# Kernel tuning notes

Measured on AMD Instinct MI355X. Metric: run time of the kernel, lower is better.

Reference implementation:

```python
import jax, jax.numpy as jnp
import numpy as np

N = 1_000_000
C = 64
B = 64
GRID = (256, 256, 256)
LEVELS = [(1, 1, 1), (2, 2, 2), (4, 4, 4), (4, 4, 8)]
NBINS_TOTAL = sum(nx * ny * nz for nx, ny, nz in LEVELS)  # 201


def setup_inputs() -> dict:
    key = jax.random.key(0)
    ks = jax.random.split(key, 12)
    feats = jax.random.normal(ks[0], (N, C), dtype=jnp.float32)
    batch_indices = jax.random.randint(ks[1], (N,), 0, B, dtype=jnp.int32)
    voxel_coords = jax.random.randint(ks[2], (N, 3), 0, 256, dtype=jnp.int32)
    s = lambda k, sh, fan: jax.random.normal(k, sh, dtype=jnp.float32) / np.sqrt(fan)
    return {
        "feats": feats,
        "batch_indices": batch_indices,
        "voxel_coords": voxel_coords,
        "batch_size": B,
        "aW1": s(ks[3], (C, 32), C), "ab1": jnp.zeros((32,), jnp.float32),
        "aW2": s(ks[4], (32, 1), 32), "ab2": jnp.zeros((1,), jnp.float32),
        "pW1": s(ks[5], (C * NBINS_TOTAL, 256), C * NBINS_TOTAL), "pb1": jnp.zeros((256,), jnp.float32),
        "pW2": s(ks[6], (256, 256), 256), "pb2": jnp.zeros((256,), jnp.float32),
    }


def _event_softmax(s, batch_indices, batch_size):
    # s: [N] raw attention scores; softmax within each event
    smax = jax.ops.segment_max(s, batch_indices, num_segments=batch_size)
    sexp = jnp.exp(s - smax[batch_indices])
    ssum = jax.ops.segment_sum(sexp, batch_indices, num_segments=batch_size)
    return sexp / (ssum[batch_indices] + 1e-8)


def reference(feats, batch_indices, voxel_coords, batch_size,
              aW1, ab1, aW2, ab2, pW1, pb1, pW2, pb2):
    # attention MLP -> per-voxel scalar score
    h = jax.nn.relu(feats @ aW1 + ab1)
    raw = (h @ aW2 + ab2)[:, 0]                       # [N]
    attn = _event_softmax(raw, batch_indices, batch_size)  # [N]
    weighted = feats * attn[:, None]                  # [N, C]

    cx = voxel_coords[:, 0].astype(jnp.float32)
    cy = voxel_coords[:, 1].astype(jnp.float32)
    cz = voxel_coords[:, 2].astype(jnp.float32)

    level_pools = []
    for nx, ny, nz in LEVELS:
        bx = jnp.clip((cx / GRID[0] * nx).astype(jnp.int32), 0, nx - 1)
        by = jnp.clip((cy / GRID[1] * ny).astype(jnp.int32), 0, ny - 1)
        bz = jnp.clip((cz / GRID[2] * nz).astype(jnp.int32), 0, nz - 1)
        bin_id = batch_indices * (nx * ny * nz) + bx * (ny * nz) + by * nz + bz
        n_bins = batch_size * nx * ny * nz
        sums = jax.ops.segment_sum(weighted, bin_id, num_segments=n_bins)      # [n_bins, C]
        counts = jax.ops.segment_sum(jnp.ones_like(bin_id, dtype=jnp.float32), bin_id,
                                     num_segments=n_bins)                      # [n_bins]
        pooled = jnp.where(counts[:, None] > 0, sums / jnp.maximum(counts, 1.0)[:, None], 0.0)
        level_pools.append(pooled.reshape(batch_size, nx * ny * nz * weighted.shape[1]))

    pyramid = jnp.concatenate(level_pools, axis=-1)   # [B, C * 201]
    return jax.nn.relu(pyramid @ pW1 + pb1) @ pW2 + pb2
```

## Files before the change

kernel.cpp:

```cpp
#include <hip/hip_runtime.h>

#define NPTS 1000000
#define C 64
#define B 64
#define NFINE 128
#define KTOT (64*201)
#define SREP 532480
#define LSTRIDE 65

typedef float f32x4 __attribute__((ext_vector_type(4)));


__global__ __launch_bounds__(256)
void zero_kernel(float4* __restrict__ p, int nf4) {
    int i = blockIdx.x * 256 + threadIdx.x;
    if (i < nf4) p[i] = make_float4(0.f, 0.f, 0.f, 0.f);
}

__global__ __launch_bounds__(256)
void fused_kernel(const float* __restrict__ feats,
                  const int* __restrict__ bidx,
                  const int* __restrict__ coords,
                  const float* __restrict__ aW1,
                  const float* __restrict__ ab1,
                  const float* __restrict__ aW2,
                  const float* __restrict__ ab2,
                  float* __restrict__ wsbase,
                  int rmask,
                  float* __restrict__ ESUM) {
    __shared__ float sh_es[B];
    __shared__ float lds_w[256 * LSTRIDE];
    float* __restrict__ S   = wsbase + (size_t)(blockIdx.x & rmask) * SREP;
    float* __restrict__ cnt = S + 524288;
    const int tid = threadIdx.x;
    const int lane = tid & 63;
    const int wv = tid >> 6;
    if (tid < B) sh_es[tid] = 0.f;
    __syncthreads();

    const int ntiles = (NPTS + 255) / 256;
    for (int tile = blockIdx.x; tile < ntiles; tile += gridDim.x) {
        const int p = tile * 256 + tid;
        int mybin = -1;
        if (p < NPTS) {
            f32x4 r[16];
            const f32x4* fr = (const f32x4*)(feats + (size_t)p * C);
            #pragma unroll
            for (int i = 0; i < 16; ++i) r[i] = __builtin_nontemporal_load(&fr[i]);
            float h[32];
            #pragma unroll
            for (int j = 0; j < 32; ++j) h[j] = ab1[j];
            #pragma unroll
            for (int i = 0; i < 16; ++i) {
                const float f0 = r[i].x, f1 = r[i].y, f2 = r[i].z, f3 = r[i].w;
                #pragma unroll
                for (int j = 0; j < 32; ++j) {
                    h[j] = fmaf(f0, aW1[(4*i+0)*32 + j],
                           fmaf(f1, aW1[(4*i+1)*32 + j],
                           fmaf(f2, aW1[(4*i+2)*32 + j],
                           fmaf(f3, aW1[(4*i+3)*32 + j], h[j]))));
                }
            }
            float raw = ab2[0];
            #pragma unroll
            for (int j = 0; j < 32; ++j) raw = fmaf(fmaxf(h[j], 0.f), aW2[j], raw);
            const float e = expf(raw);
            const int b = __builtin_nontemporal_load(&bidx[p]);
            const int cx = __builtin_nontemporal_load(&coords[3*p]);
            const int cy = __builtin_nontemporal_load(&coords[3*p+1]);
            const int cz = __builtin_nontemporal_load(&coords[3*p+2]);
            mybin = b * NFINE + ((cx >> 6) << 5) + ((cy >> 6) << 3) + (cz >> 5);
            atomicAdd(&sh_es[b], e);
            float* wr = &lds_w[tid * LSTRIDE];
            #pragma unroll
            for (int i = 0; i < 16; ++i) {
                wr[4*i+0] = r[i].x * e;
                wr[4*i+1] = r[i].y * e;
                wr[4*i+2] = r[i].z * e;
                wr[4*i+3] = r[i].w * e;
            }
        }
        #pragma unroll
        for (int q = 0; q < 64; ++q) {
            const int bq = __shfl(mybin, q);
            if (bq >= 0) {
                const float v = lds_w[(wv * 64 + q) * LSTRIDE + lane];
                atomicAdd(&S[(size_t)bq * C + lane], v);
            }
        }
        if (mybin >= 0) atomicAdd(&cnt[mybin], 1.0f);
    }
    __syncthreads();
    if (tid < B) atomicAdd(&ESUM[tid], sh_es[tid]);
}

__global__ __launch_bounds__(256)
void finalize_kernel(const float* __restrict__ wsbase, int R,
                     const float* __restrict__ ESUM, float* __restrict__ P) {
    __shared__ float sS[NFINE * C];
    __shared__ float sc[NFINE];
    const int b = blockIdx.x;
    const int tid = threadIdx.x;
    for (int i = tid; i < NFINE * C; i += 256) {
        float s = 0.f;
        for (int r = 0; r < R; ++r) s += wsbase[(size_t)r * SREP + (size_t)b * NFINE * C + i];
        sS[i] = s;
    }
    for (int i = tid; i < NFINE; i += 256) {
        float s = 0.f;
        for (int r = 0; r < R; ++r) s += wsbase[(size_t)r * SREP + 524288 + b * NFINE + i];
        sc[i] = s;
    }
    __syncthreads();
    const float inv_es = 1.0f / ESUM[b];
    float* Pb = P + (size_t)b * KTOT;
    const int lane = tid & 63;
    const int wv = tid >> 6;
    for (int bin = wv; bin < 128; bin += 4) {
        const float c = sc[bin];
        Pb[4672 + bin*C + lane] = (c > 0.f) ? sS[bin*C + lane] * inv_es / fmaxf(c, 1.f) : 0.f;
    }
    for (int bin = wv; bin < 64; bin += 4) {
        const int x = bin >> 4, y = (bin >> 2) & 3, z = bin & 3;
        const int f0 = x*32 + y*8 + 2*z;
        const float c = sc[f0] + sc[f0 + 1];
        const float s = sS[f0*C + lane] + sS[(f0+1)*C + lane];
        Pb[576 + bin*C + lane] = (c > 0.f) ? s * inv_es / fmaxf(c, 1.f) : 0.f;
    }
    for (int bin = wv; bin < 8; bin += 4) {
        const int x = bin >> 2, y = (bin >> 1) & 1, z = bin & 1;
        float c = 0.f, s = 0.f;
        for (int dx = 0; dx < 2; ++dx)
            for (int dy = 0; dy < 2; ++dy)
                for (int dz = 0; dz < 4; ++dz) {
                    const int f = (2*x+dx)*32 + (2*y+dy)*8 + (4*z+dz);
                    c += sc[f]; s += sS[f*C + lane];
                }
        Pb[64 + bin*C + lane] = (c > 0.f) ? s * inv_es / fmaxf(c, 1.f) : 0.f;
    }
    if (wv == 0) {
        float c = 0.f, s = 0.f;
        for (int f = 0; f < 128; ++f) { c += sc[f]; s += sS[f*C + lane]; }
        Pb[lane] = (c > 0.f) ? s * inv_es / fmaxf(c, 1.f) : 0.f;
    }
}

__global__ __launch_bounds__(256)
void gemm1_kernel(const float* __restrict__ P, const float* __restrict__ W1,
                  float* __restrict__ acc) {
    __shared__ float sP[64 * 128];
    const int jb = blockIdx.x;
    const int kb = blockIdx.y;
    const int k0 = kb * 128;
    const int kw = min(128, KTOT - k0);
    const int tid = threadIdx.x;
    for (int i = tid; i < 64 * 32; i += 256) {
        const int row = i >> 5, c4 = i & 31;
        if (c4 * 4 < kw)
            *(float4*)&sP[row*128 + c4*4] =
                *(const float4*)&P[(size_t)row * KTOT + k0 + c4*4];
    }
    __syncthreads();
    const int j = jb * 64 + (tid & 63);
    const int g = tid >> 6;
    float a[16];
    #pragma unroll
    for (int i = 0; i < 16; ++i) a[i] = 0.f;
    for (int k4 = 0; k4 < (kw >> 2); ++k4) {
        const int k = 4 * k4;
        const float w0 = W1[(size_t)(k0+k+0)*256 + j];
        const float w1 = W1[(size_t)(k0+k+1)*256 + j];
        const float w2 = W1[(size_t)(k0+k+2)*256 + j];
        const float w3 = W1[(size_t)(k0+k+3)*256 + j];
        #pragma unroll
        for (int i = 0; i < 16; ++i) {
            const float4 pv = *(const float4*)&sP[(g + 4*i)*128 + k];
            a[i] = fmaf(pv.x, w0, fmaf(pv.y, w1, fmaf(pv.z, w2, fmaf(pv.w, w3, a[i]))));
        }
    }
    #pragma unroll
    for (int i = 0; i < 16; ++i)
        atomicAdd(&acc[(g + 4*i)*256 + j], a[i]);
}

__global__ __launch_bounds__(256)
void gemm2_kernel(const float* __restrict__ acc, const float* __restrict__ pb1,
                  const float* __restrict__ W2, const float* __restrict__ pb2,
                  float* __restrict__ out) {
    __shared__ float R[256];
    const int b = blockIdx.x, j = threadIdx.x;
    R[j] = fmaxf(acc[b*256 + j] + pb1[j], 0.f);
    __syncthreads();
    float s = pb2[j];
    #pragma unroll 8
    for (int m = 0; m < 256; ++m) s = fmaf(R[m], W2[m*256 + j], s);
    out[b*256 + j] = s;
}

extern "C" void kernel_launch(void* const* d_in, const int* in_sizes, int n_in,
                              void* d_out, int out_size, void* d_ws, size_t ws_size,
                              hipStream_t stream) {
    const float* feats  = (const float*)d_in[0];
    const int*   bidx   = (const int*)d_in[1];
    const int*   coords = (const int*)d_in[2];
    const float* aW1 = (const float*)d_in[4];
    const float* ab1 = (const float*)d_in[5];
    const float* aW2 = (const float*)d_in[6];
    const float* ab2 = (const float*)d_in[7];
    const float* pW1 = (const float*)d_in[8];
    const float* pb1 = (const float*)d_in[9];
    const float* pW2 = (const float*)d_in[10];
    const float* pb2 = (const float*)d_in[11];
    float* out = (float*)d_out;
    float* ws  = (float*)d_ws;

    int R = 8;
    while (R > 1 && ((size_t)R * SREP + 16448 + 823296) * 4 > ws_size) R >>= 1;

    float* ESUM = ws + (size_t)R * SREP;
    float* acc1 = ESUM + 64;
    float* Pyr  = acc1 + 16384;

    const int zf4 = R * (SREP / 4) + 16448 / 4;
    hipLaunchKernelGGL(zero_kernel, dim3((zf4 + 255) / 256), dim3(256), 0, stream,
                       (float4*)ws, zf4);
    hipLaunchKernelGGL(fused_kernel, dim3(2048), dim3(256), 0, stream,
                       feats, bidx, coords, aW1, ab1, aW2, ab2, ws, R - 1, ESUM);
    hipLaunchKernelGGL(finalize_kernel, dim3(64), dim3(256), 0, stream, ws, R, ESUM, Pyr);
    hipLaunchKernelGGL(gemm1_kernel, dim3(4, 101), dim3(256), 0, stream, Pyr, pW1, acc1);
    hipLaunchKernelGGL(gemm2_kernel, dim3(64), dim3(256), 0, stream, acc1, pb1, pW2, pb2, out);
}
```

Baseline: 807.9 us.

## Pick scatter replica by XCC ID and use workgroup-scope atomics

When eight replicas are available, the fused kernel reads the hardware XCC ID and picks the partial-sum replica private to that chiplet. It then issues relaxed workgroup-scope float atomics, so the adds can resolve in that XCC's L2 instead of at device coherence scope. The LDS staging buffer is also halved by processing each wavefront's 64 points in two 32-point halves, which lowers shared-memory use per block and may allow more resident blocks. The risk is correctness: it relies on all blocks of one XCC sharing an L2 and on results being written back at kernel end.

```diff
diff --git a/kernel.cpp b/kernel.cpp
--- a/kernel.cpp
+++ b/kernel.cpp
@@ -17,6 +17,7 @@
     if (i < nf4) p[i] = make_float4(0.f, 0.f, 0.f, 0.f);
 }
 
+template<int LOCAL>
 __global__ __launch_bounds__(256)
 void fused_kernel(const float* __restrict__ feats,
                   const int* __restrict__ bidx,
@@ -29,8 +30,16 @@
                   int rmask,
                   float* __restrict__ ESUM) {
     __shared__ float sh_es[B];
-    __shared__ float lds_w[256 * LSTRIDE];
-    float* __restrict__ S   = wsbase + (size_t)(blockIdx.x & rmask) * SREP;
+    __shared__ float lds_w[128 * LSTRIDE];
+    int rep;
+    if (LOCAL) {
+        unsigned int xcc;
+        asm volatile("s_getreg_b32 %0, hwreg(HW_REG_XCC_ID)" : "=s"(xcc));
+        rep = (int)(xcc & 7u);
+    } else {
+        rep = blockIdx.x & rmask;
+    }
+    float* __restrict__ S   = wsbase + (size_t)rep * SREP;
     float* __restrict__ cnt = S + 524288;
     const int tid = threadIdx.x;
     const int lane = tid & 63;
@@ -42,8 +51,9 @@
     for (int tile = blockIdx.x; tile < ntiles; tile += gridDim.x) {
         const int p = tile * 256 + tid;
         int mybin = -1;
+        f32x4 r[16];
+        float e = 0.f;
         if (p < NPTS) {
-            f32x4 r[16];
             const f32x4* fr = (const f32x4*)(feats + (size_t)p * C);
             #pragma unroll
             for (int i = 0; i < 16; ++i) r[i] = __builtin_nontemporal_load(&fr[i]);
@@ -64,31 +74,46 @@
             float raw = ab2[0];
             #pragma unroll
             for (int j = 0; j < 32; ++j) raw = fmaf(fmaxf(h[j], 0.f), aW2[j], raw);
-            const float e = expf(raw);
+            e = expf(raw);
             const int b = __builtin_nontemporal_load(&bidx[p]);
             const int cx = __builtin_nontemporal_load(&coords[3*p]);
             const int cy = __builtin_nontemporal_load(&coords[3*p+1]);
             const int cz = __builtin_nontemporal_load(&coords[3*p+2]);
             mybin = b * NFINE + ((cx >> 6) << 5) + ((cy >> 6) << 3) + (cz >> 5);
             atomicAdd(&sh_es[b], e);
-            float* wr = &lds_w[tid * LSTRIDE];
-            #pragma unroll
-            for (int i = 0; i < 16; ++i) {
-                wr[4*i+0] = r[i].x * e;
-                wr[4*i+1] = r[i].y * e;
-                wr[4*i+2] = r[i].z * e;
-                wr[4*i+3] = r[i].w * e;
+        }
+        #pragma unroll
+        for (int sub = 0; sub < 2; ++sub) {
+            if (mybin >= 0 && (lane >> 5) == sub) {
+                float* wr = &lds_w[(wv * 32 + (lane & 31)) * LSTRIDE];
+                #pragma unroll
+                for (int i = 0; i < 16; ++i) {
+                    wr[4*i+0] = r[i].x * e;
+                    wr[4*i+1] = r[i].y * e;
+                    wr[4*i+2] = r[i].z * e;
+                    wr[4*i+3] = r[i].w * e;
+                }
             }
-        }
-        #pragma unroll
-        for (int q = 0; q < 64; ++q) {
-            const int bq = __shfl(mybin, q);
-            if (bq >= 0) {
-                const float v = lds_w[(wv * 64 + q) * LSTRIDE + lane];
-                atomicAdd(&S[(size_t)bq * C + lane], v);
+            #pragma unroll
+            for (int q = 0; q < 32; ++q) {
+                const int bq = __shfl(mybin, sub * 32 + q);
+                if (bq >= 0) {
+                    const float v = lds_w[(wv * 32 + q) * LSTRIDE + lane];
+                    if (LOCAL)
+                        __hip_atomic_fetch_add(&S[(size_t)bq * C + lane], v,
+                                               __ATOMIC_RELAXED, __HIP_MEMORY_SCOPE_WORKGROUP);
+                    else
+                        atomicAdd(&S[(size_t)bq * C + lane], v);
+                }
             }
         }
-        if (mybin >= 0) atomicAdd(&cnt[mybin], 1.0f);
+        if (mybin >= 0) {
+            if (LOCAL)
+                __hip_atomic_fetch_add(&cnt[mybin], 1.0f,
+                                       __ATOMIC_RELAXED, __HIP_MEMORY_SCOPE_WORKGROUP);
+            else
+                atomicAdd(&cnt[mybin], 1.0f);
+        }
     }
     __syncthreads();
     if (tid < B) atomicAdd(&ESUM[tid], sh_es[tid]);
@@ -224,8 +249,12 @@
     const int zf4 = R * (SREP / 4) + 16448 / 4;
     hipLaunchKernelGGL(zero_kernel, dim3((zf4 + 255) / 256), dim3(256), 0, stream,
                        (float4*)ws, zf4);
-    hipLaunchKernelGGL(fused_kernel, dim3(2048), dim3(256), 0, stream,
-                       feats, bidx, coords, aW1, ab1, aW2, ab2, ws, R - 1, ESUM);
+    if (R == 8)
+        hipLaunchKernelGGL((fused_kernel<1>), dim3(2048), dim3(256), 0, stream,
+                           feats, bidx, coords, aW1, ab1, aW2, ab2, ws, 7, ESUM);
+    else
+        hipLaunchKernelGGL((fused_kernel<0>), dim3(2048), dim3(256), 0, stream,
+                           feats, bidx, coords, aW1, ab1, aW2, ab2, ws, R - 1, ESUM);
     hipLaunchKernelGGL(finalize_kernel, dim3(64), dim3(256), 0, stream, ws, R, ESUM, Pyr);
     hipLaunchKernelGGL(gemm1_kernel, dim3(4, 101), dim3(256), 0, stream, Pyr, pW1, acc1);
     hipLaunchKernelGGL(gemm2_kernel, dim3(64), dim3(256), 0, stream, acc1, pb1, pW2, pb2, out);
```

New measurement: 808.3 us. About the same (+0.1%).

## Replace atomic scatter pooling with counting-sort by bin and segmented gather-reduce

Applied to the files above, without the earlier changes.

The fused MLP-plus-atomic-scatter kernel is split up. An MLP pass writes each point's exp score and fine bin id. A histogram, three scan kernels and a placement kernel then counting-sort the point indices by bin, and a gather kernel reduces each bin's features with no atomics. This removes the heavy global float atomics and the replicated accumulation buffers. In exchange it adds a second random-access read of the 256MB feats array, several small serial kernels (a single-block scan, 64-block hist/place), and extra launches.

```diff
diff --git a/kernel.cpp b/kernel.cpp
--- a/kernel.cpp
+++ b/kernel.cpp
@@ -3,114 +3,187 @@
 #define NPTS 1000000
 #define C 64
 #define B 64
-#define NFINE 128
+#define NBINS 8192
 #define KTOT (64*201)
-#define SREP 532480
-#define LSTRIDE 65
+#define NSLICE 64
+#define SLICE 15625
+#define A 1048576
 
 typedef float f32x4 __attribute__((ext_vector_type(4)));
 
-
-__global__ __launch_bounds__(256)
-void zero_kernel(float4* __restrict__ p, int nf4) {
+#define ZOFF (4*A + 1056800)
+
+__global__ __launch_bounds__(256)
+void zero_kernel(float4* __restrict__ p) {
     int i = blockIdx.x * 256 + threadIdx.x;
-    if (i < nf4) p[i] = make_float4(0.f, 0.f, 0.f, 0.f);
-}
-
-__global__ __launch_bounds__(256)
-void fused_kernel(const float* __restrict__ feats,
-                  const int* __restrict__ bidx,
-                  const int* __restrict__ coords,
-                  const float* __restrict__ aW1,
-                  const float* __restrict__ ab1,
-                  const float* __restrict__ aW2,
-                  const float* __restrict__ ab2,
-                  float* __restrict__ wsbase,
-                  int rmask,
-                  float* __restrict__ ESUM) {
+    if (i < 16448 / 4) p[i] = make_float4(0.f, 0.f, 0.f, 0.f);
+}
+
+__global__ __launch_bounds__(256)
+void mlp_kernel(const float* __restrict__ feats,
+                const int* __restrict__ bidx,
+                const int* __restrict__ coords,
+                const float* __restrict__ aW1,
+                const float* __restrict__ ab1,
+                const float* __restrict__ aW2,
+                const float* __restrict__ ab2,
+                float* __restrict__ earr,
+                int* __restrict__ binarr,
+                float* __restrict__ ESUM) {
     __shared__ float sh_es[B];
-    __shared__ float lds_w[256 * LSTRIDE];
-    float* __restrict__ S   = wsbase + (size_t)(blockIdx.x & rmask) * SREP;
-    float* __restrict__ cnt = S + 524288;
-    const int tid = threadIdx.x;
-    const int lane = tid & 63;
-    const int wv = tid >> 6;
+    const int tid = threadIdx.x;
     if (tid < B) sh_es[tid] = 0.f;
     __syncthreads();
-
-    const int ntiles = (NPTS + 255) / 256;
-    for (int tile = blockIdx.x; tile < ntiles; tile += gridDim.x) {
-        const int p = tile * 256 + tid;
-        int mybin = -1;
-        if (p < NPTS) {
-            f32x4 r[16];
-            const f32x4* fr = (const f32x4*)(feats + (size_t)p * C);
+    for (int p = blockIdx.x * 256 + tid; p < NPTS; p += gridDim.x * 256) {
+        f32x4 r[16];
+        const f32x4* fr = (const f32x4*)(feats + (size_t)p * C);
+        #pragma unroll
+        for (int i = 0; i < 16; ++i) r[i] = __builtin_nontemporal_load(&fr[i]);
+        float h[32];
+        #pragma unroll
+        for (int j = 0; j < 32; ++j) h[j] = ab1[j];
+        #pragma unroll
+        for (int i = 0; i < 16; ++i) {
+            const float f0 = r[i].x, f1 = r[i].y, f2 = r[i].z, f3 = r[i].w;
             #pragma unroll
-            for (int i = 0; i < 16; ++i) r[i] = __builtin_nontemporal_load(&fr[i]);
-            float h[32];
-            #pragma unroll
-            for (int j = 0; j < 32; ++j) h[j] = ab1[j];
-            #pragma unroll
-            for (int i = 0; i < 16; ++i) {
-                const float f0 = r[i].x, f1 = r[i].y, f2 = r[i].z, f3 = r[i].w;
-                #pragma unroll
-                for (int j = 0; j < 32; ++j) {
-                    h[j] = fmaf(f0, aW1[(4*i+0)*32 + j],
-                           fmaf(f1, aW1[(4*i+1)*32 + j],
-                           fmaf(f2, aW1[(4*i+2)*32 + j],
-                           fmaf(f3, aW1[(4*i+3)*32 + j], h[j]))));
-                }
-            }
-            float raw = ab2[0];
-            #pragma unroll
-            for (int j = 0; j < 32; ++j) raw = fmaf(fmaxf(h[j], 0.f), aW2[j], raw);
-            const float e = expf(raw);
-            const int b = __builtin_nontemporal_load(&bidx[p]);
-            const int cx = __builtin_nontemporal_load(&coords[3*p]);
-            const int cy = __builtin_nontemporal_load(&coords[3*p+1]);
-            const int cz = __builtin_nontemporal_load(&coords[3*p+2]);
-            mybin = b * NFINE + ((cx >> 6) << 5) + ((cy >> 6) << 3) + (cz >> 5);
-            atomicAdd(&sh_es[b], e);
-            float* wr = &lds_w[tid * LSTRIDE];
-            #pragma unroll
-            for (int i = 0; i < 16; ++i) {
-                wr[4*i+0] = r[i].x * e;
-                wr[4*i+1] = r[i].y * e;
-                wr[4*i+2] = r[i].z * e;
-                wr[4*i+3] = r[i].w * e;
+            for (int j = 0; j < 32; ++j) {
+                h[j] = fmaf(f0, aW1[(4*i+0)*32 + j],
+                       fmaf(f1, aW1[(4*i+1)*32 + j],
+                       fmaf(f2, aW1[(4*i+2)*32 + j],
+                       fmaf(f3, aW1[(4*i+3)*32 + j], h[j]))));
             }
         }
-        #pragma unroll
-        for (int q = 0; q < 64; ++q) {
-            const int bq = __shfl(mybin, q);
-            if (bq >= 0) {
-                const float v = lds_w[(wv * 64 + q) * LSTRIDE + lane];
-                atomicAdd(&S[(size_t)bq * C + lane], v);
-            }
+        float raw = ab2[0];
+        #pragma unroll
+        for (int j = 0; j < 32; ++j) raw = fmaf(fmaxf(h[j], 0.f), aW2[j], raw);
+        const float e = expf(raw);
+        const int b  = __builtin_nontemporal_load(&bidx[p]);
+        const int cx = __builtin_nontemporal_load(&coords[3*p]);
+        const int cy = __builtin_nontemporal_load(&coords[3*p+1]);
+        const int cz = __builtin_nontemporal_load(&coords[3*p+2]);
+        earr[p]   = e;
+        binarr[p] = b * 128 + ((cx >> 6) << 5) + ((cy >> 6) << 3) + (cz >> 5);
+        atomicAdd(&sh_es[b], e);
+    }
+    __syncthreads();
+    if (tid < B) atomicAdd(&ESUM[tid], sh_es[tid]);
+}
+
+__global__ __launch_bounds__(256)
+void hist_kernel(const int* __restrict__ binarr, int* __restrict__ hist2d) {
+    __shared__ int h[NBINS];
+    const int tid = threadIdx.x;
+    for (int i = tid; i < NBINS; i += 256) h[i] = 0;
+    __syncthreads();
+    const int lo = blockIdx.x * SLICE, hi = lo + SLICE;
+    for (int p = lo + tid; p < hi; p += 256) atomicAdd(&h[binarr[p]], 1);
+    __syncthreads();
+    for (int i = tid; i < NBINS; i += 256) hist2d[blockIdx.x * NBINS + i] = h[i];
+}
+
+__global__ __launch_bounds__(256)
+void scanA_kernel(const int* __restrict__ hist2d, int* __restrict__ binstart) {
+    const int gid = blockIdx.x * 256 + threadIdx.x;
+    if (gid < NBINS) {
+        int s = 0;
+        for (int b = 0; b < NSLICE; ++b) s += hist2d[b * NBINS + gid];
+        binstart[gid] = s;
+    }
+}
+
+__global__ __launch_bounds__(256)
+void scanB_kernel(int* __restrict__ binstart) {
+    __shared__ int c[NBINS];
+    __shared__ int part[257];
+    const int tid = threadIdx.x;
+    for (int i = tid; i < NBINS; i += 256) c[i] = binstart[i];
+    __syncthreads();
+    const int base = tid * 32;
+    int s = 0;
+    #pragma unroll
+    for (int j = 0; j < 32; ++j) s += c[base + j];
+    part[tid + 1] = s;
+    if (tid == 0) part[0] = 0;
+    __syncthreads();
+    if (tid == 0) for (int i = 1; i <= 256; ++i) part[i] += part[i - 1];
+    __syncthreads();
+    int off = part[tid];
+    #pragma unroll
+    for (int j = 0; j < 32; ++j) { const int t = c[base + j]; binstart[base + j] = off; off += t; }
+    if (tid == 255) binstart[NBINS] = off;
+}
+
+__global__ __launch_bounds__(256)
+void scanC_kernel(const int* __restrict__ hist2d, const int* __restrict__ binstart,
+                  int* __restrict__ offs2d) {
+    const int gid = blockIdx.x * 256 + threadIdx.x;
+    if (gid < NBINS) {
+        int off = binstart[gid];
+        for (int b = 0; b < NSLICE; ++b) {
+            offs2d[b * NBINS + gid] = off;
+            off += hist2d[b * NBINS + gid];
         }
-        if (mybin >= 0) atomicAdd(&cnt[mybin], 1.0f);
-    }
-    __syncthreads();
-    if (tid < B) atomicAdd(&ESUM[tid], sh_es[tid]);
-}
-
-__global__ __launch_bounds__(256)
-void finalize_kernel(const float* __restrict__ wsbase, int R,
+    }
+}
+
+__global__ __launch_bounds__(256)
+void place_kernel(const int* __restrict__ binarr, const float* __restrict__ earr,
+                  const int* __restrict__ offs2d,
+                  int* __restrict__ sidx, float* __restrict__ sexp) {
+    __shared__ int cur[NBINS];
+    const int tid = threadIdx.x;
+    for (int i = tid; i < NBINS; i += 256) cur[i] = offs2d[blockIdx.x * NBINS + i];
+    __syncthreads();
+    const int lo = blockIdx.x * SLICE, hi = lo + SLICE;
+    for (int p = lo + tid; p < hi; p += 256) {
+        const int b = binarr[p];
+        const int pos = atomicAdd(&cur[b], 1);
+        sidx[pos] = p;
+        sexp[pos] = earr[p];
+    }
+}
+
+__global__ __launch_bounds__(256)
+void reduce_kernel(const float* __restrict__ feats,
+                   const int* __restrict__ sidx, const float* __restrict__ sexp,
+                   const int* __restrict__ binstart, float* __restrict__ S) {
+    const int tid = threadIdx.x;
+    const int lane = tid & 63;
+    const int bin = blockIdx.x * 4 + (tid >> 6);
+    const int start = binstart[bin], end = binstart[bin + 1];
+    float a0 = 0.f, a1 = 0.f, a2 = 0.f, a3 = 0.f;
+    int k = start;
+    for (; k + 3 < end; k += 4) {
+        const int i0 = sidx[k],     i1 = sidx[k + 1];
+        const int i2 = sidx[k + 2], i3 = sidx[k + 3];
+        const float e0 = sexp[k],     e1 = sexp[k + 1];
+        const float e2 = sexp[k + 2], e3 = sexp[k + 3];
+        const float v0 = __builtin_nontemporal_load(feats + (size_t)i0 * C + lane);
+        const float v1 = __builtin_nontemporal_load(feats + (size_t)i1 * C + lane);
+        const float v2 = __builtin_nontemporal_load(feats + (size_t)i2 * C + lane);
+        const float v3 = __builtin_nontemporal_load(feats + (size_t)i3 * C + lane);
+        a0 = fmaf(v0, e0, a0);
+        a1 = fmaf(v1, e1, a1);
+        a2 = fmaf(v2, e2, a2);
+        a3 = fmaf(v3, e3, a3);
+    }
+    for (; k < end; ++k) {
+        const float v = __builtin_nontemporal_load(feats + (size_t)sidx[k] * C + lane);
+        a0 = fmaf(v, sexp[k], a0);
+    }
+    S[(size_t)bin * C + lane] = (a0 + a1) + (a2 + a3);
+}
+
+__global__ __launch_bounds__(256)
+void finalize_kernel(const float* __restrict__ S, const int* __restrict__ binstart,
                      const float* __restrict__ ESUM, float* __restrict__ P) {
-    __shared__ float sS[NFINE * C];
-    __shared__ float sc[NFINE];
+    __shared__ float sS[128 * C];
+    __shared__ float sc[128];
     const int b = blockIdx.x;
     const int tid = threadIdx.x;
-    for (int i = tid; i < NFINE * C; i += 256) {
-        float s = 0.f;
-        for (int r = 0; r < R; ++r) s += wsbase[(size_t)r * SREP + (size_t)b * NFINE * C + i];
-        sS[i] = s;
-    }
-    for (int i = tid; i < NFINE; i += 256) {
-        float s = 0.f;
-        for (int r = 0; r < R; ++r) s += wsbase[(size_t)r * SREP + 524288 + b * NFINE + i];
-        sc[i] = s;
-    }
+    for (int i = tid; i < 128 * C; i += 256) sS[i] = S[(size_t)b * 128 * C + i];
+    for (int i = tid; i < 128; i += 256)
+        sc[i] = (float)(binstart[b * 128 + i + 1] - binstart[b * 128 + i]);
     __syncthreads();
     const float inv_es = 1.0f / ESUM[b];
     float* Pb = P + (size_t)b * KTOT;
@@ -214,19 +287,30 @@
     float* out = (float*)d_out;
     float* ws  = (float*)d_ws;
 
-    int R = 8;
-    while (R > 1 && ((size_t)R * SREP + 16448 + 823296) * 4 > ws_size) R >>= 1;
-
-    float* ESUM = ws + (size_t)R * SREP;
-    float* acc1 = ESUM + 64;
-    float* Pyr  = acc1 + 16384;
-
-    const int zf4 = R * (SREP / 4) + 16448 / 4;
-    hipLaunchKernelGGL(zero_kernel, dim3((zf4 + 255) / 256), dim3(256), 0, stream,
-                       (float4*)ws, zf4);
-    hipLaunchKernelGGL(fused_kernel, dim3(2048), dim3(256), 0, stream,
-                       feats, bidx, coords, aW1, ab1, aW2, ab2, ws, R - 1, ESUM);
-    hipLaunchKernelGGL(finalize_kernel, dim3(64), dim3(256), 0, stream, ws, R, ESUM, Pyr);
+    int*   binarr   = (int*)ws;
+    float* earr     = ws + A;
+    int*   sidx     = (int*)(ws + 2*A);
+    float* sexp     = ws + 3*A;
+    int*   hist2d   = (int*)(ws + 4*A);
+    int*   offs2d   = (int*)(ws + 4*A + 524288);
+    int*   binstart = (int*)(ws + 4*A + 1048576);
+    float* ESUM     = ws + ZOFF;
+    float* acc1     = ESUM + 64;
+    float* S        = ws;
+    float* Pyr      = ws + A;
+
+    hipLaunchKernelGGL(zero_kernel, dim3(17), dim3(256), 0, stream, (float4*)(ws + ZOFF));
+    hipLaunchKernelGGL(mlp_kernel, dim3(2048), dim3(256), 0, stream,
+                       feats, bidx, coords, aW1, ab1, aW2, ab2, earr, binarr, ESUM);
+    hipLaunchKernelGGL(hist_kernel, dim3(NSLICE), dim3(256), 0, stream, binarr, hist2d);
+    hipLaunchKernelGGL(scanA_kernel, dim3(32), dim3(256), 0, stream, hist2d, binstart);
+    hipLaunchKernelGGL(scanB_kernel, dim3(1), dim3(256), 0, stream, binstart);
+    hipLaunchKernelGGL(scanC_kernel, dim3(32), dim3(256), 0, stream, hist2d, binstart, offs2d);
+    hipLaunchKernelGGL(place_kernel, dim3(NSLICE), dim3(256), 0, stream,
+                       binarr, earr, offs2d, sidx, sexp);
+    hipLaunchKernelGGL(reduce_kernel, dim3(2048), dim3(256), 0, stream,
+                       feats, sidx, sexp, binstart, S);
+    hipLaunchKernelGGL(finalize_kernel, dim3(64), dim3(256), 0, stream, S, binstart, ESUM, Pyr);
     hipLaunchKernelGGL(gemm1_kernel, dim3(4, 101), dim3(256), 0, stream, Pyr, pW1, acc1);
     hipLaunchKernelGGL(gemm2_kernel, dim3(64), dim3(256), 0, stream, acc1, pb1, pW2, pb2, out);
 }
```

After: 739.4 us. -8.5%, faster.
